# Optimization experiments

Hardware: AMD Instinct MI355X
Metric: run time of the kernel (lower is better)

Reference implementation:

```python
import jax, jax.numpy as jnp
from jax import lax
import numpy as np


def setup_inputs() -> dict:
    key = jax.random.key(0)
    ks = jax.random.split(key, 8)
    B, Cin, H, W = 4, 64, 128, 128
    D, N = 2 * Cin, 64  # D = in_ch*2, N = ssd_state_dim*2
    s = np.float32(1.0 / np.sqrt(D))
    return {
        "x": jax.random.normal(ks[0], (B, Cin, H, W), jnp.float32),
        "h_prev": jnp.zeros((B, D, N), jnp.float32),
        "norm_w": jnp.ones((D,), jnp.float32),
        "norm_b": jnp.zeros((D,), jnp.float32),
        "W_x": jax.random.normal(ks[1], (D, D), jnp.float32) * s,
        "W_B": jax.random.normal(ks[2], (N, D), jnp.float32) * s,
        "W_C": jax.random.normal(ks[3], (N, D), jnp.float32) * s,
        "w_dt": jax.random.normal(ks[4], (D,), jnp.float32) * s,
        "dt_bias": jnp.float32(0.0),
        "A_log": jnp.float32(0.0),
        "D_skip": jax.random.normal(ks[5], (D,), jnp.float32),
        "W_out": jax.random.normal(ks[6], (D, D), jnp.float32) * s,
    }


def _forward(x, h_prev, norm_w, norm_b, W_x, W_B, W_C, w_dt, dt_bias, A_log, D_skip, W_out):
    B, C, H, W = x.shape
    # rfft2 -> complex [B, C, Hf, Wf]
    xf = jnp.fft.rfft2(x, norm='ortho')
    Hf, Wf = xf.shape[-2], xf.shape[-1]
    L = Hf * Wf
    sqrt_n = jnp.sqrt(jnp.float32(H * W))
    # pack real/imag along channels: [B, 2C, L]
    u = jnp.concatenate([xf.real.reshape(B, C, L), xf.imag.reshape(B, C, L)], axis=1)
    # LayerNorm1D over the channel dim
    mu = jnp.mean(u, axis=1, keepdims=True)
    var = jnp.var(u, axis=1, keepdims=True)
    u = (u - mu) * lax.rsqrt(var + 1e-5) * norm_w[None, :, None] + norm_b[None, :, None]
    u = u / sqrt_n
    # SSD (Mamba2-style) recurrence over the L frequency tokens
    xs = jnp.einsum('ed,bdl->lbe', W_x, u)   # [L, B, D]
    Bs = jnp.einsum('nd,bdl->lbn', W_B, u)   # [L, B, N]
    Cs = jnp.einsum('nd,bdl->lbn', W_C, u)   # [L, B, N]
    dt = jax.nn.softplus(jnp.einsum('d,bdl->lb', w_dt, u) + dt_bias)  # [L, B]
    dec = jnp.exp(-jnp.exp(A_log) * dt)       # [L, B], A = -exp(A_log)

    def step(h, inp):
        x_t, B_t, C_t, dec_t, dt_t = inp
        h = dec_t[:, None, None] * h + (dt_t[:, None] * x_t)[:, :, None] * B_t[:, None, :]
        y_t = jnp.einsum('bdn,bn->bd', h, C_t)
        return h, y_t

    h_last, ys = lax.scan(step, h_prev, (xs, Bs, Cs, dec, dt))  # ys [L, B, D]
    y = ys.transpose(1, 2, 0) + D_skip[None, :, None] * xs.transpose(1, 2, 0)  # [B, D, L]
    freq_out = jnp.einsum('ed,bdl->bel', W_out, y) * sqrt_n
    # unpack real/imag halves and inverse FFT
    ft = (freq_out[:, :C] + 1j * freq_out[:, C:]).reshape(B, C, Hf, Wf)
    y_sp = jnp.fft.irfft2(ft, s=(H, W), norm='ortho')
    return y_sp, h_last


def reference(x, h_prev, norm_w, norm_b, W_x, W_B, W_C, w_dt, dt_bias, A_log, D_skip, W_out):
    return _forward(x, h_prev, norm_w, norm_b, W_x, W_B, W_C, w_dt, dt_bias, A_log, D_skip, W_out)
```

## Files before the change

kernel.cpp:

```cpp
#include <hip/hip_runtime.h>
#include <hip/hip_bf16.h>
#include <math.h>

#define BB 4
#define CC 64
#define HH 128
#define WW 128
#define DD 128
#define NN 64
#define HF 128
#define WF 65
#define LL 8320
#define TSEG 64
#define NSEG 130
#define PI2f 6.283185307179586f

__device__ __forceinline__ int brev7(int x) { return (int)(__brev((unsigned)x) >> 25); }

__global__ void k0_transpose(const float* __restrict__ Wx, const float* __restrict__ Wb,
                             const float* __restrict__ Wc, const float* __restrict__ Wout,
                             float* __restrict__ WcatT, float* __restrict__ WoT) {
  int idx = blockIdx.x * 256 + threadIdx.x;
  if (idx < 128 * 256) {
    int k = idx >> 8, o = idx & 255;
    float v;
    if (o < 128)      v = Wx[o * 128 + k];
    else if (o < 192) v = Wb[(o - 128) * 128 + k];
    else              v = Wc[(o - 192) * 128 + k];
    WcatT[k * 256 + o] = v;
  }
  if (idx < 128 * 128) {
    int d = idx >> 7, e = idx & 127;
    WoT[d * 128 + e] = Wout[e * 128 + d];
  }
}

__global__ __launch_bounds__(256) void k1_rfft(const float* __restrict__ x,
                                               float* __restrict__ T1) {
  __shared__ float2 data[128 * 17];
  __shared__ float2 tw[64];
  int tid = threadIdx.x;
  if (tid < 64) {
    float sv, cv;
    sincosf(PI2f * (float)tid * (1.f / 128.f), &sv, &cv);
    tw[tid] = make_float2(cv, sv);
  }
  int r0 = blockIdx.x * 32;
  const float* xp = x + (size_t)r0 * 128;
#pragma unroll
  for (int i = 0; i < 8; i++) {
    int e = i * 256 + tid;
    int p = e >> 7, j = e & 127;
    float v1 = xp[(2 * p) * 128 + j];
    float v2 = xp[(2 * p + 1) * 128 + j];
    data[brev7(j) * 17 + p] = make_float2(v1, v2);
  }
  __syncthreads();
  for (int s = 1; s <= 7; s++) {
    int half = 1 << (s - 1);
    int tsh = 7 - s;
#pragma unroll
    for (int i = 0; i < 4; i++) {
      int idx = i * 256 + tid;
      int t = idx >> 4, c = idx & 15;
      int j = t & (half - 1);
      int pos = ((t >> (s - 1)) << s) + j;
      float2 a = data[pos * 17 + c];
      float2 b = data[(pos + half) * 17 + c];
      float2 w = tw[j << tsh];
      float2 m = make_float2(b.x * w.x + b.y * w.y, b.y * w.x - b.x * w.y);
      data[pos * 17 + c] = make_float2(a.x + m.x, a.y + m.y);
      data[(pos + half) * 17 + c] = make_float2(a.x - m.x, a.y - m.y);
    }
    __syncthreads();
  }
  const float inv = 1.f / 128.f;
  float2* o = (float2*)T1 + (size_t)r0 * 65;
#pragma unroll
  for (int i = 0; i < 5; i++) {
    int e = i * 256 + tid;
    if (e < 1040) {
      int p = e / 65, k = e - p * 65;
      float2 Z = data[k * 17 + p];
      float2 Zc = data[((128 - k) & 127) * 17 + p];
      float2 X1 = make_float2((Z.x + Zc.x) * 0.5f * inv, (Z.y - Zc.y) * 0.5f * inv);
      float2 X2 = make_float2((Z.y + Zc.y) * 0.5f * inv, (Zc.x - Z.x) * 0.5f * inv);
      o[(2 * p) * 65 + k] = X1;
      o[(2 * p + 1) * 65 + k] = X2;
    }
  }
}

__global__ __launch_bounds__(256) void k2a_fft(const float* __restrict__ T1,
                                               float* __restrict__ uT) {
  __shared__ float2 data[128 * 34];
  __shared__ float2 tw[64];
  int tid = threadIdx.x;
  if (tid < 64) {
    float sv, cv;
    sincosf(PI2f * (float)tid * (1.f / 128.f), &sv, &cv);
    tw[tid] = make_float2(cv, sv);
  }
  int chunk = blockIdx.x & 1;
  int bc = blockIdx.x >> 1;
  int wf0 = chunk * 32;
  const float2* Tp = (const float2*)T1 + (size_t)bc * 8320;
#pragma unroll
  for (int i = 0; i < 17; i++) {
    int e = i * 256 + tid;
    if (e < 4224) {
      int j = e / 33;
      int c = e - j * 33;
      data[brev7(j) * 34 + c] = Tp[j * 65 + wf0 + c];
    }
  }
  __syncthreads();
  for (int s = 1; s <= 7; s++) {
    int half = 1 << (s - 1);
    int tsh = 7 - s;
#pragma unroll
    for (int i = 0; i < 9; i++) {
      int idx = i * 256 + tid;
      if (idx < 2112) {
        int t = idx / 33;
        int c = idx - t * 33;
        int j = t & (half - 1);
        int pos = ((t >> (s - 1)) << s) + j;
        float2 a = data[pos * 34 + c];
        float2 b = data[(pos + half) * 34 + c];
        float2 w = tw[j << tsh];
        float2 m = make_float2(b.x * w.x + b.y * w.y, b.y * w.x - b.x * w.y);
        data[pos * 34 + c] = make_float2(a.x + m.x, a.y + m.y);
        data[(pos + half) * 34 + c] = make_float2(a.x - m.x, a.y - m.y);
      }
    }
    __syncthreads();
  }
  int b = bc >> 6, ch = bc & 63;
  float* pr = uT + (size_t)(b * 128 + ch) * 8320;
  float* pi = uT + (size_t)(b * 128 + 64 + ch) * 8320;
#pragma unroll
  for (int i = 0; i < 17; i++) {
    int e = i * 256 + tid;
    if (e < 4224) {
      int hf = e / 33;
      int c = e - hf * 33;
      float2 v = data[hf * 34 + c];
      pr[hf * 65 + wf0 + c] = v.x;
      pi[hf * 65 + wf0 + c] = v.y;
    }
  }
}

__global__ __launch_bounds__(256) void k3_ln_proj(
    const float* __restrict__ uT, const float* __restrict__ WcatT,
    const float* __restrict__ nw, const float* __restrict__ nb,
    const float* __restrict__ wdt, const float* __restrict__ dtbias,
    float* __restrict__ xs, float* __restrict__ Bs, float* __restrict__ Cs,
    float* __restrict__ dtb) {
  __shared__ float su[128 * 65];
  __shared__ float snw[128], snb[128], swdt[128];
  int tid = threadIdx.x;
  int b = blockIdx.x / 130, tile = blockIdx.x % 130;
  int l0 = tile * 64;
  if (tid < 128) { snw[tid] = nw[tid]; snb[tid] = nb[tid]; swdt[tid] = wdt[tid]; }
  const float* up = uT + (size_t)b * 128 * 8320 + l0;
#pragma unroll
  for (int i = 0; i < 8; i++) {
    int e = i * 256 + tid;
    int d = e >> 4, q = e & 15;
    float4 v = *(const float4*)(up + (size_t)d * 8320 + q * 4);
    su[d * 65 + q * 4 + 0] = v.x; su[d * 65 + q * 4 + 1] = v.y;
    su[d * 65 + q * 4 + 2] = v.z; su[d * 65 + q * 4 + 3] = v.w;
  }
  __syncthreads();
  int t = tid >> 2, j = tid & 3;
  float vals[32];
  float s = 0.f, s2 = 0.f;
#pragma unroll
  for (int i = 0; i < 32; i++) {
    float v = su[(4 * i + j) * 65 + t];
    vals[i] = v; s += v; s2 += v * v;
  }
  s += __shfl_xor(s, 1, 64);  s += __shfl_xor(s, 2, 64);
  s2 += __shfl_xor(s2, 1, 64); s2 += __shfl_xor(s2, 2, 64);
  float mu = s * (1.f / 128.f);
  float var = s2 * (1.f / 128.f) - mu * mu;
  float rs = rsqrtf(var + 1e-5f);
  float raw = 0.f;
#pragma unroll
  for (int i = 0; i < 32; i++) {
    int k = 4 * i + j;
    float v = ((vals[i] - mu) * rs * snw[k] + snb[k]) * (1.f / 128.f);
    su[k * 65 + t] = v;
    raw = fmaf(v, swdt[k], raw);
  }
  raw += __shfl_xor(raw, 1, 64); raw += __shfl_xor(raw, 2, 64);
  if (j == 0) {
    float z = raw + dtbias[0];
    float sp = fmaxf(z, 0.f) + log1pf(expf(-fabsf(z)));
    dtb[b * LL + l0 + t] = sp;
  }
  __syncthreads();
  int wv = tid >> 6;
  int lane = tid & 63;
  int t0 = wv * 16;
  float acc[16][4];
#pragma unroll
  for (int i = 0; i < 16; i++)
#pragma unroll
    for (int r = 0; r < 4; r++) acc[i][r] = 0.f;
  const float4* W4 = (const float4*)WcatT;
  for (int k = 0; k < 128; k++) {
    float4 w = W4[k * 64 + lane];
    const float* sr = &su[k * 65 + t0];
#pragma unroll
    for (int i = 0; i < 16; i++) {
      float uk = sr[i];
      acc[i][0] = fmaf(w.x, uk, acc[i][0]);
      acc[i][1] = fmaf(w.y, uk, acc[i][1]);
      acc[i][2] = fmaf(w.z, uk, acc[i][2]);
      acc[i][3] = fmaf(w.w, uk, acc[i][3]);
    }
  }
  size_t tok0 = (size_t)b * LL + l0 + t0;
  float* basep;
  size_t stride;
  if (lane < 32)      { basep = xs + tok0 * 128 + lane * 4;        stride = 128; }
  else if (lane < 48) { basep = Bs + tok0 * 64 + (lane - 32) * 4;  stride = 64; }
  else                { basep = Cs + tok0 * 64 + (lane - 48) * 4;  stride = 64; }
#pragma unroll
  for (int i = 0; i < 16; i++)
    *(float4*)(basep + (size_t)i * stride) =
        make_float4(acc[i][0], acc[i][1], acc[i][2], acc[i][3]);
}

__global__ __launch_bounds__(256) void k5_seg(
    const float* __restrict__ xs, const float* __restrict__ Bs, const float* __restrict__ Cs,
    const float* __restrict__ dtb, const float* __restrict__ Alog,
    const float* __restrict__ Dskip,
    float* __restrict__ ybuf, float* __restrict__ Sseg, float* __restrict__ ssegb,
    float* __restrict__ cumg) {
  __shared__ __align__(16) float sX[64 * 128];
  __shared__ __align__(16) float sB[64 * 68];
  __shared__ __align__(16) float sCM[64 * 68];
  __shared__ float sdt[64], slc[64], sws[64];
  int tid = threadIdx.x;
  int b = blockIdx.x / NSEG, seg = blockIdx.x % NSEG;
  int tokbase = b * LL + seg * TSEG;
  const float4* xg = (const float4*)(xs + (size_t)tokbase * 128);
  float4* sX4 = (float4*)sX;
#pragma unroll
  for (int i = 0; i < 8; i++) sX4[i * 256 + tid] = xg[i * 256 + tid];
  const float4* bg = (const float4*)(Bs + (size_t)tokbase * 64);
  const float4* cg = (const float4*)(Cs + (size_t)tokbase * 64);
#pragma unroll
  for (int i = 0; i < 4; i++) {
    int e = i * 256 + tid;
    int t = e >> 4, n4 = e & 15;
    *(float4*)&sB[t * 68 + n4 * 4] = bg[e];
    *(float4*)&sCM[t * 68 + n4 * 4] = cg[e];
  }
  if (tid < 64) sdt[tid] = dtb[tokbase + tid];
  __syncthreads();
  if (tid < 64) {
    float a = expf(Alog[0]);
    float v = -a * sdt[tid];
#pragma unroll
    for (int off = 1; off < 64; off <<= 1) {
      float o = __shfl_up(v, off, 64);
      if (tid >= off) v += o;
    }
    slc[tid] = v;
    float l63 = __shfl(v, 63, 64);
    sws[tid] = expf(l63 - v) * sdt[tid];
    cumg[tokbase + tid] = expf(v);
    if (tid == 63) ssegb[seg * BB + b] = expf(v);
  }
  __syncthreads();
  int t0 = (tid >> 4) * 4, s0 = (tid & 15) * 4;
  float g[4][4];
#pragma unroll
  for (int i = 0; i < 4; i++)
#pragma unroll
    for (int j = 0; j < 4; j++) g[i][j] = 0.f;
  for (int n4 = 0; n4 < 16; n4++) {
    float4 cr[4], br[4];
#pragma unroll
    for (int i = 0; i < 4; i++) cr[i] = *(const float4*)&sCM[(t0 + i) * 68 + n4 * 4];
#pragma unroll
    for (int j = 0; j < 4; j++) br[j] = *(const float4*)&sB[(s0 + j) * 68 + n4 * 4];
#pragma unroll
    for (int i = 0; i < 4; i++)
#pragma unroll
      for (int j = 0; j < 4; j++) {
        g[i][j] = fmaf(cr[i].x, br[j].x, g[i][j]);
        g[i][j] = fmaf(cr[i].y, br[j].y, g[i][j]);
        g[i][j] = fmaf(cr[i].z, br[j].z, g[i][j]);
        g[i][j] = fmaf(cr[i].w, br[j].w, g[i][j]);
      }
  }
  __syncthreads();
#pragma unroll
  for (int i = 0; i < 4; i++) {
    int t = t0 + i;
    float4 m;
    float lt = slc[t];
    m.x = (s0 + 0 <= t) ? expf(lt - slc[s0 + 0]) * sdt[s0 + 0] * g[i][0] : 0.f;
    m.y = (s0 + 1 <= t) ? expf(lt - slc[s0 + 1]) * sdt[s0 + 1] * g[i][1] : 0.f;
    m.z = (s0 + 2 <= t) ? expf(lt - slc[s0 + 2]) * sdt[s0 + 2] * g[i][2] : 0.f;
    m.w = (s0 + 3 <= t) ? expf(lt - slc[s0 + 3]) * sdt[s0 + 3] * g[i][3] : 0.f;
    *(float4*)&sCM[t * 68 + s0] = m;
  }
  __syncthreads();
  int d0 = (tid & 15) * 8;
  {
    float acc[4][8];
#pragma unroll
    for (int i = 0; i < 4; i++)
#pragma unroll
      for (int j = 0; j < 8; j++) acc[i][j] = 0.f;
    for (int s = 0; s < 64; s++) {
      float4 x0 = *(const float4*)&sX[s * 128 + d0];
      float4 x1 = *(const float4*)&sX[s * 128 + d0 + 4];
      float xv[8] = {x0.x, x0.y, x0.z, x0.w, x1.x, x1.y, x1.z, x1.w};
#pragma unroll
      for (int i = 0; i < 4; i++) {
        float m = sCM[(t0 + i) * 68 + s];
#pragma unroll
        for (int j = 0; j < 8; j++) acc[i][j] = fmaf(m, xv[j], acc[i][j]);
      }
    }
    float4 dk0 = *(const float4*)&Dskip[d0];
    float4 dk1 = *(const float4*)&Dskip[d0 + 4];
    float dk[8] = {dk0.x, dk0.y, dk0.z, dk0.w, dk1.x, dk1.y, dk1.z, dk1.w};
#pragma unroll
    for (int i = 0; i < 4; i++) {
      int t = t0 + i;
      float4 x0 = *(const float4*)&sX[t * 128 + d0];
      float4 x1 = *(const float4*)&sX[t * 128 + d0 + 4];
      float xv[8] = {x0.x, x0.y, x0.z, x0.w, x1.x, x1.y, x1.z, x1.w};
      float4 y0, y1;
      y0.x = fmaf(dk[0], xv[0], acc[i][0]); y0.y = fmaf(dk[1], xv[1], acc[i][1]);
      y0.z = fmaf(dk[2], xv[2], acc[i][2]); y0.w = fmaf(dk[3], xv[3], acc[i][3]);
      y1.x = fmaf(dk[4], xv[4], acc[i][4]); y1.y = fmaf(dk[5], xv[5], acc[i][5]);
      y1.z = fmaf(dk[6], xv[6], acc[i][6]); y1.w = fmaf(dk[7], xv[7], acc[i][7]);
      float* yp = ybuf + (size_t)(tokbase + t) * 128 + d0;
      *(float4*)yp = y0;
      *(float4*)(yp + 4) = y1;
    }
  }
  {
    int dd0 = (tid >> 4) * 8, n0 = (tid & 15) * 4;
    float sacc[8][4];
#pragma unroll
    for (int k = 0; k < 8; k++)
#pragma unroll
      for (int j = 0; j < 4; j++) sacc[k][j] = 0.f;
    for (int s = 0; s < 64; s++) {
      float w = sws[s];
      float4 b4 = *(const float4*)&sB[s * 68 + n0];
      b4.x *= w; b4.y *= w; b4.z *= w; b4.w *= w;
      float4 x0 = *(const float4*)&sX[s * 128 + dd0];
      float4 x1 = *(const float4*)&sX[s * 128 + dd0 + 4];
      float xv[8] = {x0.x, x0.y, x0.z, x0.w, x1.x, x1.y, x1.z, x1.w};
#pragma unroll
      for (int k = 0; k < 8; k++) {
        sacc[k][0] = fmaf(xv[k], b4.x, sacc[k][0]);
        sacc[k][1] = fmaf(xv[k], b4.y, sacc[k][1]);
        sacc[k][2] = fmaf(xv[k], b4.z, sacc[k][2]);
        sacc[k][3] = fmaf(xv[k], b4.w, sacc[k][3]);
      }
    }
    float* Sp = Sseg + (size_t)seg * 32768 + (size_t)b * 8192;
#pragma unroll
    for (int k = 0; k < 8; k++)
      *(float4*)&Sp[(dd0 + k) * 64 + n0] =
          make_float4(sacc[k][0], sacc[k][1], sacc[k][2], sacc[k][3]);
  }
}

__global__ void k5b_states(const float* __restrict__ h_prev, const float* __restrict__ Sseg,
                           const float* __restrict__ ssegb, float* __restrict__ Hp,
                           float* __restrict__ h_last) {
  int gid = blockIdx.x * 256 + threadIdx.x;
  int b = gid >> 13;
  float h = h_prev[gid];
  for (int p = 0; p < NSEG; p++) {
    Hp[(size_t)p * 32768 + gid] = h;
    h = fmaf(ssegb[p * 4 + b], h, Sseg[(size_t)p * 32768 + gid]);
  }
  h_last[gid] = h;
}

__global__ __launch_bounds__(256) void k5c_correct(
    const float* __restrict__ Cs, const float* __restrict__ Hp,
    const float* __restrict__ cumg, float* __restrict__ ybuf) {
  __shared__ __align__(16) float Ct[64 * 64];
  __shared__ __align__(16) float Ht[64 * 132];
  __shared__ float cg[64];
  int tid = threadIdx.x;
  int b = blockIdx.x / NSEG, seg = blockIdx.x % NSEG;
  int tokbase = b * LL + seg * 64;
  const float* Csrc = Cs + (size_t)tokbase * 64;
#pragma unroll
  for (int i = 0; i < 16; i++) {
    int e = tid + i * 256;
    Ct[(e & 63) * 64 + (e >> 6)] = Csrc[e];
  }
  const float* Hsrc = Hp + (size_t)seg * 32768 + (size_t)b * 8192;
#pragma unroll
  for (int i = 0; i < 32; i++) {
    int e = tid + i * 256;
    Ht[(e & 63) * 132 + (e >> 6)] = Hsrc[e];
  }
  if (tid < 64) cg[tid] = cumg[tokbase + tid];
  __syncthreads();
  int og = tid & 15, tg = tid >> 4;
  int d0 = og * 8, t0 = tg * 4;
  float acc[4][8];
#pragma unroll
  for (int i = 0; i < 4; i++)
#pragma unroll
    for (int jj = 0; jj < 8; jj++) acc[i][jj] = 0.f;
  for (int n = 0; n < 64; n++) {
    float4 c4 = *(const float4*)&Ct[n * 64 + t0];
    float4 h0 = *(const float4*)&Ht[n * 132 + d0];
    float4 h1 = *(const float4*)&Ht[n * 132 + d0 + 4];
    float cv[4] = {c4.x, c4.y, c4.z, c4.w};
    float hv[8] = {h0.x, h0.y, h0.z, h0.w, h1.x, h1.y, h1.z, h1.w};
#pragma unroll
    for (int i = 0; i < 4; i++)
#pragma unroll
      for (int jj = 0; jj < 8; jj++) acc[i][jj] = fmaf(cv[i], hv[jj], acc[i][jj]);
  }
#pragma unroll
  for (int i = 0; i < 4; i++) {
    float sc = cg[t0 + i];
    float* yp = ybuf + (size_t)(tokbase + t0 + i) * 128 + d0;
    float4 y0 = *(float4*)yp;
    float4 y1 = *(float4*)(yp + 4);
    y0.x = fmaf(sc, acc[i][0], y0.x); y0.y = fmaf(sc, acc[i][1], y0.y);
    y0.z = fmaf(sc, acc[i][2], y0.z); y0.w = fmaf(sc, acc[i][3], y0.w);
    y1.x = fmaf(sc, acc[i][4], y1.x); y1.y = fmaf(sc, acc[i][5], y1.y);
    y1.z = fmaf(sc, acc[i][6], y1.z); y1.w = fmaf(sc, acc[i][7], y1.w);
    *(float4*)yp = y0; *(float4*)(yp + 4) = y1;
  }
}

__global__ __launch_bounds__(256) void k6_outproj(
    const float* __restrict__ ybuf, const float* __restrict__ WoT,
    float* __restrict__ T2) {
  __shared__ float sy[128 * 65];
  int tid = threadIdx.x;
  int b = blockIdx.x / 130, tile = blockIdx.x % 130;
  int l0 = tile * 64;
  const float* yg = ybuf + ((size_t)b * LL + l0) * 128;
#pragma unroll
  for (int i = 0; i < 8; i++) {
    int e = i * 256 + tid;
    int t = e >> 5, q = e & 31;
    float4 v = *(const float4*)(yg + t * 128 + q * 4);
    sy[(q * 4 + 0) * 65 + t] = v.x; sy[(q * 4 + 1) * 65 + t] = v.y;
    sy[(q * 4 + 2) * 65 + t] = v.z; sy[(q * 4 + 3) * 65 + t] = v.w;
  }
  __syncthreads();
  int wv = tid >> 6;
  int lane = tid & 63;
  int o4 = lane & 31, th = lane >> 5;
  int tt0 = wv * 16 + th * 8;
  float acc[8][4];
#pragma unroll
  for (int i = 0; i < 8; i++)
#pragma unroll
    for (int r = 0; r < 4; r++) acc[i][r] = 0.f;
  const float4* W4 = (const float4*)WoT;
  for (int k = 0; k < 128; k++) {
    float4 w = W4[k * 32 + o4];
    const float* sr = &sy[k * 65 + tt0];
#pragma unroll
    for (int i = 0; i < 8; i++) {
      float yk = sr[i];
      acc[i][0] = fmaf(w.x, yk, acc[i][0]);
      acc[i][1] = fmaf(w.y, yk, acc[i][1]);
      acc[i][2] = fmaf(w.z, yk, acc[i][2]);
      acc[i][3] = fmaf(w.w, yk, acc[i][3]);
    }
  }
#pragma unroll
  for (int i = 0; i < 8; i++) {
    int l = l0 + tt0 + i;
    *(float4*)(T2 + ((size_t)b * LL + l) * 128 + o4 * 4) =
        make_float4(acc[i][0] * 128.f, acc[i][1] * 128.f,
                    acc[i][2] * 128.f, acc[i][3] * 128.f);
  }
}

__global__ __launch_bounds__(256) void k7t_transpose(const float* __restrict__ T2,
                                                     float* __restrict__ T2T) {
  __shared__ __align__(16) float tile[32][132];
  int tid = threadIdx.x;
  int b = blockIdx.x / 260, lt = blockIdx.x % 260;
  int l0 = lt * 32;
#pragma unroll
  for (int i = 0; i < 4; i++) {
    int e = i * 256 + tid;
    int l = e >> 5, f4 = e & 31;
    float4 v = *(const float4*)(T2 + ((size_t)(b * LL + l0 + l)) * 128 + f4 * 4);
    *(float4*)&tile[l][f4 * 4] = v;
  }
  __syncthreads();
  int l = tid & 31, c2 = tid >> 5;
  float2* out = (float2*)T2T;
#pragma unroll
  for (int k = 0; k < 8; k++) {
    int c = c2 * 8 + k;
    float2 z = make_float2(tile[l][c], tile[l][64 + c]);
    out[((size_t)(b * 64 + c)) * 8320 + l0 + l] = z;
  }
}

__global__ __launch_bounds__(256) void k7a_fft(const float* __restrict__ T2T,
                                               float* __restrict__ TY) {
  __shared__ float2 data[128 * 34];
  __shared__ float2 tw[64];
  int tid = threadIdx.x;
  if (tid < 64) {
    float sv, cv;
    sincosf(PI2f * (float)tid * (1.f / 128.f), &sv, &cv);
    tw[tid] = make_float2(cv, sv);
  }
  int chunk = blockIdx.x & 1;
  int bc = blockIdx.x >> 1;
  int wf0 = chunk * 32;
  const float2* Zp = (const float2*)T2T + (size_t)bc * 8320;
#pragma unroll
  for (int i = 0; i < 17; i++) {
    int e = i * 256 + tid;
    if (e < 4224) {
      int j = e / 33;
      int c = e - j * 33;
      data[brev7(j) * 34 + c] = Zp[j * 65 + wf0 + c];
    }
  }
  __syncthreads();
  for (int s = 1; s <= 7; s++) {
    int half = 1 << (s - 1);
    int tsh = 7 - s;
#pragma unroll
    for (int i = 0; i < 9; i++) {
      int idx = i * 256 + tid;
      if (idx < 2112) {
        int t = idx / 33;
        int c = idx - t * 33;
        int j = t & (half - 1);
        int pos = ((t >> (s - 1)) << s) + j;
        float2 a = data[pos * 34 + c];
        float2 b = data[(pos + half) * 34 + c];
        float2 w = tw[j << tsh];
        float2 m = make_float2(b.x * w.x - b.y * w.y, b.y * w.x + b.x * w.y);
        data[pos * 34 + c] = make_float2(a.x + m.x, a.y + m.y);
        data[(pos + half) * 34 + c] = make_float2(a.x - m.x, a.y - m.y);
      }
    }
    __syncthreads();
  }
  float2* po = (float2*)TY + (size_t)bc * 8320;
#pragma unroll
  for (int i = 0; i < 17; i++) {
    int e = i * 256 + tid;
    if (e < 4224) {
      int h = e / 33;
      int c = e - h * 33;
      po[h * 65 + wf0 + c] = data[h * 34 + c];
    }
  }
}

__global__ __launch_bounds__(256) void k8_irfft(const float* __restrict__ TY,
                                                float* __restrict__ out) {
  __shared__ float2 zsh[32 * 66];
  __shared__ float2 data[128 * 17];
  __shared__ float2 tw[64];
  int tid = threadIdx.x;
  if (tid < 64) {
    float sv, cv;
    sincosf(PI2f * (float)tid * (1.f / 128.f), &sv, &cv);
    tw[tid] = make_float2(cv, sv);
  }
  int r0 = blockIdx.x * 32;
  const float2* Zp = (const float2*)TY + (size_t)r0 * 65;
#pragma unroll
  for (int i = 0; i < 9; i++) {
    int e = i * 256 + tid;
    if (e < 2080) {
      int r = e / 65, wf = e - r * 65;
      zsh[r * 66 + wf] = Zp[r * 65 + wf];
    }
  }
  __syncthreads();
#pragma unroll
  for (int i = 0; i < 8; i++) {
    int e = i * 256 + tid;
    int p = e >> 7, j = e & 127;
    int jj = (j <= 64) ? j : 128 - j;
    float2 a1 = zsh[(2 * p) * 66 + jj];
    float2 a2 = zsh[(2 * p + 1) * 66 + jj];
    if (jj == 0 || jj == 64) { a1.y = 0.f; a2.y = 0.f; }
    float2 V = (j <= 64) ? make_float2(a1.x - a2.y, a1.y + a2.x)
                         : make_float2(a1.x + a2.y, a2.x - a1.y);
    data[brev7(j) * 17 + p] = V;
  }
  __syncthreads();
  for (int s = 1; s <= 7; s++) {
    int half = 1 << (s - 1);
    int tsh = 7 - s;
#pragma unroll
    for (int i = 0; i < 4; i++) {
      int idx = i * 256 + tid;
      int t = idx >> 4, c = idx & 15;
      int j = t & (half - 1);
      int pos = ((t >> (s - 1)) << s) + j;
      float2 a = data[pos * 17 + c];
      float2 b = data[(pos + half) * 17 + c];
      float2 w = tw[j << tsh];
      float2 m = make_float2(b.x * w.x - b.y * w.y, b.y * w.x + b.x * w.y);
      data[pos * 17 + c] = make_float2(a.x + m.x, a.y + m.y);
      data[(pos + half) * 17 + c] = make_float2(a.x - m.x, a.y - m.y);
    }
    __syncthreads();
  }
  const float inv = 1.f / 128.f;
  float* op = out + (size_t)r0 * 128;
#pragma unroll
  for (int i = 0; i < 8; i++) {
    int e = i * 256 + tid;
    int p = e >> 7, w = e & 127;
    float2 X = data[w * 17 + p];
    op[(2 * p) * 128 + w] = X.x * inv;
    op[(2 * p + 1) * 128 + w] = X.y * inv;
  }
}

extern "C" void kernel_launch(void* const* d_in, const int* in_sizes, int n_in,
                              void* d_out, int out_size, void* d_ws, size_t ws_size,
                              hipStream_t stream) {
  const float* x      = (const float*)d_in[0];
  const float* h_prev = (const float*)d_in[1];
  const float* nw     = (const float*)d_in[2];
  const float* nb     = (const float*)d_in[3];
  const float* Wx     = (const float*)d_in[4];
  const float* Wb     = (const float*)d_in[5];
  const float* Wc     = (const float*)d_in[6];
  const float* wdt    = (const float*)d_in[7];
  const float* dtbias = (const float*)d_in[8];
  const float* Alog   = (const float*)d_in[9];
  const float* Dskip  = (const float*)d_in[10];
  const float* Wout   = (const float*)d_in[11];
  float* out = (float*)d_out;

  float* ws = (float*)d_ws;
  const size_t SZ_BIG = 4259840;
  const size_t SZ_BN  = 2129920;
  float* RA = ws;
  float* RB = RA + SZ_BIG;
  float* RC = RB + SZ_BIG;
  float* RD = RC + SZ_BIG;
  float* RE = RD + SZ_BN;
  float* dtb   = RE + SZ_BN;
  float* cumg  = dtb + 33280;
  float* ssegb = cumg + 33280;
  float* WcatT = ssegb + 520;
  float* WoT   = WcatT + 32768;

  hipLaunchKernelGGL(k0_transpose, dim3(128), dim3(256), 0, stream, Wx, Wb, Wc, Wout, WcatT, WoT);
  hipLaunchKernelGGL(k1_rfft, dim3(1024), dim3(256), 0, stream, x, RA );
  hipLaunchKernelGGL(k2a_fft, dim3(512), dim3(256), 0, stream, RA , RB );
  hipLaunchKernelGGL(k3_ln_proj, dim3(520), dim3(256), 0, stream,
                     RB , WcatT, nw, nb, wdt, dtbias, RA , RD , RE , dtb);
  hipLaunchKernelGGL(k5_seg, dim3(520), dim3(256), 0, stream,
                     RA , RD , RE , dtb, Alog, Dskip,
                     RB , RC , ssegb, cumg);
  hipLaunchKernelGGL(k5b_states, dim3(128), dim3(256), 0, stream,
                     h_prev, RC , ssegb, RA , out + 4194304);
  hipLaunchKernelGGL(k5c_correct, dim3(520), dim3(256), 0, stream,
                     RE , RA , cumg, RB );
  hipLaunchKernelGGL(k6_outproj, dim3(520), dim3(256), 0, stream, RB , WoT, RC );
  hipLaunchKernelGGL(k7t_transpose, dim3(1040), dim3(256), 0, stream, RC , RD );
  hipLaunchKernelGGL(k7a_fft, dim3(512), dim3(256), 0, stream, RD , RA );
  hipLaunchKernelGGL(k8_irfft, dim3(1024), dim3(256), 0, stream, RA , out);
}
```

Measured before the change: 212.6 us.

## Split segment kernel over D halves and vectorize shared-memory reads in projections

The segment-scan kernel now launches twice as many blocks, each handling half of the D channels, which halves per-block shared memory and register accumulators. The Gram matrix and decay computations are duplicated across the two halves in exchange for more parallelism across CUs. The LN-projection and out-projection kernels change their shared-memory padding from 65 to 68 floats so that inner-loop reads become float4 loads, and they add a min-blocks-per-CU launch bound of 2. The padding of 68 may bring back bank conflicts on transposed scalar accesses, and the duplicated Gram work adds compute.

Measured after the change: 211.8 us. About the same (-0.4%).

```diff
diff --git a/kernel.cpp b/kernel.cpp
--- a/kernel.cpp
+++ b/kernel.cpp
@@ -152,13 +152,13 @@
   }
 }
 
-__global__ __launch_bounds__(256) void k3_ln_proj(
+__global__ __launch_bounds__(256, 2) void k3_ln_proj(
     const float* __restrict__ uT, const float* __restrict__ WcatT,
     const float* __restrict__ nw, const float* __restrict__ nb,
     const float* __restrict__ wdt, const float* __restrict__ dtbias,
     float* __restrict__ xs, float* __restrict__ Bs, float* __restrict__ Cs,
     float* __restrict__ dtb) {
-  __shared__ float su[128 * 65];
+  __shared__ float su[128 * 68];
   __shared__ float snw[128], snb[128], swdt[128];
   int tid = threadIdx.x;
   int b = blockIdx.x / 130, tile = blockIdx.x % 130;
@@ -170,8 +170,7 @@
     int e = i * 256 + tid;
     int d = e >> 4, q = e & 15;
     float4 v = *(const float4*)(up + (size_t)d * 8320 + q * 4);
-    su[d * 65 + q * 4 + 0] = v.x; su[d * 65 + q * 4 + 1] = v.y;
-    su[d * 65 + q * 4 + 2] = v.z; su[d * 65 + q * 4 + 3] = v.w;
+    *(float4*)&su[d * 68 + q * 4] = v;
   }
   __syncthreads();
   int t = tid >> 2, j = tid & 3;
@@ -179,7 +178,7 @@
   float s = 0.f, s2 = 0.f;
 #pragma unroll
   for (int i = 0; i < 32; i++) {
-    float v = su[(4 * i + j) * 65 + t];
+    float v = su[(4 * i + j) * 68 + t];
     vals[i] = v; s += v; s2 += v * v;
   }
   s += __shfl_xor(s, 1, 64);  s += __shfl_xor(s, 2, 64);
@@ -192,7 +191,7 @@
   for (int i = 0; i < 32; i++) {
     int k = 4 * i + j;
     float v = ((vals[i] - mu) * rs * snw[k] + snb[k]) * (1.f / 128.f);
-    su[k * 65 + t] = v;
+    su[k * 68 + t] = v;
     raw = fmaf(v, swdt[k], raw);
   }
   raw += __shfl_xor(raw, 1, 64); raw += __shfl_xor(raw, 2, 64);
@@ -213,14 +212,16 @@
   const float4* W4 = (const float4*)WcatT;
   for (int k = 0; k < 128; k++) {
     float4 w = W4[k * 64 + lane];
-    const float* sr = &su[k * 65 + t0];
+    const float4* sr4 = (const float4*)&su[k * 68 + t0];
+    float4 u0 = sr4[0], u1 = sr4[1], u2 = sr4[2], u3 = sr4[3];
+    float uk[16] = {u0.x, u0.y, u0.z, u0.w, u1.x, u1.y, u1.z, u1.w,
+                    u2.x, u2.y, u2.z, u2.w, u3.x, u3.y, u3.z, u3.w};
 #pragma unroll
     for (int i = 0; i < 16; i++) {
-      float uk = sr[i];
-      acc[i][0] = fmaf(w.x, uk, acc[i][0]);
-      acc[i][1] = fmaf(w.y, uk, acc[i][1]);
-      acc[i][2] = fmaf(w.z, uk, acc[i][2]);
-      acc[i][3] = fmaf(w.w, uk, acc[i][3]);
+      acc[i][0] = fmaf(w.x, uk[i], acc[i][0]);
+      acc[i][1] = fmaf(w.y, uk[i], acc[i][1]);
+      acc[i][2] = fmaf(w.z, uk[i], acc[i][2]);
+      acc[i][3] = fmaf(w.w, uk[i], acc[i][3]);
     }
   }
   size_t tok0 = (size_t)b * LL + l0 + t0;
@@ -241,17 +242,22 @@
     const float* __restrict__ Dskip,
     float* __restrict__ ybuf, float* __restrict__ Sseg, float* __restrict__ ssegb,
     float* __restrict__ cumg) {
-  __shared__ __align__(16) float sX[64 * 128];
+  __shared__ __align__(16) float sX[64 * 68];
   __shared__ __align__(16) float sB[64 * 68];
   __shared__ __align__(16) float sCM[64 * 68];
   __shared__ float sdt[64], slc[64], sws[64];
   int tid = threadIdx.x;
-  int b = blockIdx.x / NSEG, seg = blockIdx.x % NSEG;
+  int half = blockIdx.x & 1;
+  int bs = blockIdx.x >> 1;
+  int b = bs / NSEG, seg = bs % NSEG;
   int tokbase = b * LL + seg * TSEG;
   const float4* xg = (const float4*)(xs + (size_t)tokbase * 128);
-  float4* sX4 = (float4*)sX;
-#pragma unroll
-  for (int i = 0; i < 8; i++) sX4[i * 256 + tid] = xg[i * 256 + tid];
+#pragma unroll
+  for (int i = 0; i < 4; i++) {
+    int e = i * 256 + tid;
+    int t = e >> 4, q = e & 15;
+    *(float4*)&sX[t * 68 + q * 4] = xg[t * 32 + half * 16 + q];
+  }
   const float4* bg = (const float4*)(Bs + (size_t)tokbase * 64);
   const float4* cg = (const float4*)(Cs + (size_t)tokbase * 64);
 #pragma unroll
@@ -274,8 +280,10 @@
     slc[tid] = v;
     float l63 = __shfl(v, 63, 64);
     sws[tid] = expf(l63 - v) * sdt[tid];
-    cumg[tokbase + tid] = expf(v);
-    if (tid == 63) ssegb[seg * BB + b] = expf(v);
+    if (half == 0) {
+      cumg[tokbase + tid] = expf(v);
+      if (tid == 63) ssegb[seg * BB + b] = expf(v);
+    }
   }
   __syncthreads();
   int t0 = (tid >> 4) * 4, s0 = (tid & 15) * 4;
@@ -313,69 +321,62 @@
     *(float4*)&sCM[t * 68 + s0] = m;
   }
   __syncthreads();
-  int d0 = (tid & 15) * 8;
   {
-    float acc[4][8];
+    int d0 = (tid & 15) * 4;
+    float acc[4][4];
 #pragma unroll
     for (int i = 0; i < 4; i++)
 #pragma unroll
-      for (int j = 0; j < 8; j++) acc[i][j] = 0.f;
+      for (int j = 0; j < 4; j++) acc[i][j] = 0.f;
     for (int s = 0; s < 64; s++) {
-      float4 x0 = *(const float4*)&sX[s * 128 + d0];
-      float4 x1 = *(const float4*)&sX[s * 128 + d0 + 4];
-      float xv[8] = {x0.x, x0.y, x0.z, x0.w, x1.x, x1.y, x1.z, x1.w};
+      float4 xv = *(const float4*)&sX[s * 68 + d0];
 #pragma unroll
       for (int i = 0; i < 4; i++) {
         float m = sCM[(t0 + i) * 68 + s];
-#pragma unroll
-        for (int j = 0; j < 8; j++) acc[i][j] = fmaf(m, xv[j], acc[i][j]);
+        acc[i][0] = fmaf(m, xv.x, acc[i][0]);
+        acc[i][1] = fmaf(m, xv.y, acc[i][1]);
+        acc[i][2] = fmaf(m, xv.z, acc[i][2]);
+        acc[i][3] = fmaf(m, xv.w, acc[i][3]);
       }
     }
-    float4 dk0 = *(const float4*)&Dskip[d0];
-    float4 dk1 = *(const float4*)&Dskip[d0 + 4];
-    float dk[8] = {dk0.x, dk0.y, dk0.z, dk0.w, dk1.x, dk1.y, dk1.z, dk1.w};
+    float4 dk = *(const float4*)&Dskip[half * 64 + d0];
 #pragma unroll
     for (int i = 0; i < 4; i++) {
       int t = t0 + i;
-      float4 x0 = *(const float4*)&sX[t * 128 + d0];
-      float4 x1 = *(const float4*)&sX[t * 128 + d0 + 4];
-      float xv[8] = {x0.x, x0.y, x0.z, x0.w, x1.x, x1.y, x1.z, x1.w};
-      float4 y0, y1;
-      y0.x = fmaf(dk[0], xv[0], acc[i][0]); y0.y = fmaf(dk[1], xv[1], acc[i][1]);
-      y0.z = fmaf(dk[2], xv[2], acc[i][2]); y0.w = fmaf(dk[3], xv[3], acc[i][3]);
-      y1.x = fmaf(dk[4], xv[4], acc[i][4]); y1.y = fmaf(dk[5], xv[5], acc[i][5]);
-      y1.z = fmaf(dk[6], xv[6], acc[i][6]); y1.w = fmaf(dk[7], xv[7], acc[i][7]);
-      float* yp = ybuf + (size_t)(tokbase + t) * 128 + d0;
-      *(float4*)yp = y0;
-      *(float4*)(yp + 4) = y1;
+      float4 xv = *(const float4*)&sX[t * 68 + d0];
+      float4 y;
+      y.x = fmaf(dk.x, xv.x, acc[i][0]);
+      y.y = fmaf(dk.y, xv.y, acc[i][1]);
+      y.z = fmaf(dk.z, xv.z, acc[i][2]);
+      y.w = fmaf(dk.w, xv.w, acc[i][3]);
+      *(float4*)(ybuf + (size_t)(tokbase + t) * 128 + half * 64 + d0) = y;
     }
   }
   {
-    int dd0 = (tid >> 4) * 8, n0 = (tid & 15) * 4;
-    float sacc[8][4];
-#pragma unroll
-    for (int k = 0; k < 8; k++)
+    int dd0 = (tid >> 4) * 4, n0 = (tid & 15) * 4;
+    float sacc[4][4];
+#pragma unroll
+    for (int k = 0; k < 4; k++)
 #pragma unroll
       for (int j = 0; j < 4; j++) sacc[k][j] = 0.f;
     for (int s = 0; s < 64; s++) {
       float w = sws[s];
       float4 b4 = *(const float4*)&sB[s * 68 + n0];
       b4.x *= w; b4.y *= w; b4.z *= w; b4.w *= w;
-      float4 x0 = *(const float4*)&sX[s * 128 + dd0];
-      float4 x1 = *(const float4*)&sX[s * 128 + dd0 + 4];
-      float xv[8] = {x0.x, x0.y, x0.z, x0.w, x1.x, x1.y, x1.z, x1.w};
-#pragma unroll
-      for (int k = 0; k < 8; k++) {
-        sacc[k][0] = fmaf(xv[k], b4.x, sacc[k][0]);
-        sacc[k][1] = fmaf(xv[k], b4.y, sacc[k][1]);
-        sacc[k][2] = fmaf(xv[k], b4.z, sacc[k][2]);
-        sacc[k][3] = fmaf(xv[k], b4.w, sacc[k][3]);
+      float4 xv = *(const float4*)&sX[s * 68 + dd0];
+      float xk[4] = {xv.x, xv.y, xv.z, xv.w};
+#pragma unroll
+      for (int k = 0; k < 4; k++) {
+        sacc[k][0] = fmaf(xk[k], b4.x, sacc[k][0]);
+        sacc[k][1] = fmaf(xk[k], b4.y, sacc[k][1]);
+        sacc[k][2] = fmaf(xk[k], b4.z, sacc[k][2]);
+        sacc[k][3] = fmaf(xk[k], b4.w, sacc[k][3]);
       }
     }
     float* Sp = Sseg + (size_t)seg * 32768 + (size_t)b * 8192;
 #pragma unroll
-    for (int k = 0; k < 8; k++)
-      *(float4*)&Sp[(dd0 + k) * 64 + n0] =
+    for (int k = 0; k < 4; k++)
+      *(float4*)&Sp[(half * 64 + dd0 + k) * 64 + n0] =
           make_float4(sacc[k][0], sacc[k][1], sacc[k][2], sacc[k][3]);
   }
 }
@@ -448,10 +449,10 @@
   }
 }
 
-__global__ __launch_bounds__(256) void k6_outproj(
+__global__ __launch_bounds__(256, 2) void k6_outproj(
     const float* __restrict__ ybuf, const float* __restrict__ WoT,
     float* __restrict__ T2) {
-  __shared__ float sy[128 * 65];
+  __shared__ float sy[128 * 68];
   int tid = threadIdx.x;
   int b = blockIdx.x / 130, tile = blockIdx.x % 130;
   int l0 = tile * 64;
@@ -461,8 +462,8 @@
     int e = i * 256 + tid;
     int t = e >> 5, q = e & 31;
     float4 v = *(const float4*)(yg + t * 128 + q * 4);
-    sy[(q * 4 + 0) * 65 + t] = v.x; sy[(q * 4 + 1) * 65 + t] = v.y;
-    sy[(q * 4 + 2) * 65 + t] = v.z; sy[(q * 4 + 3) * 65 + t] = v.w;
+    sy[(q * 4 + 0) * 68 + t] = v.x; sy[(q * 4 + 1) * 68 + t] = v.y;
+    sy[(q * 4 + 2) * 68 + t] = v.z; sy[(q * 4 + 3) * 68 + t] = v.w;
   }
   __syncthreads();
   int wv = tid >> 6;
@@ -477,14 +478,15 @@
   const float4* W4 = (const float4*)WoT;
   for (int k = 0; k < 128; k++) {
     float4 w = W4[k * 32 + o4];
-    const float* sr = &sy[k * 65 + tt0];
+    const float4* sr4 = (const float4*)&sy[k * 68 + tt0];
+    float4 u0 = sr4[0], u1 = sr4[1];
+    float yk[8] = {u0.x, u0.y, u0.z, u0.w, u1.x, u1.y, u1.z, u1.w};
 #pragma unroll
     for (int i = 0; i < 8; i++) {
-      float yk = sr[i];
-      acc[i][0] = fmaf(w.x, yk, acc[i][0]);
-      acc[i][1] = fmaf(w.y, yk, acc[i][1]);
-      acc[i][2] = fmaf(w.z, yk, acc[i][2]);
-      acc[i][3] = fmaf(w.w, yk, acc[i][3]);
+      acc[i][0] = fmaf(w.x, yk[i], acc[i][0]);
+      acc[i][1] = fmaf(w.y, yk[i], acc[i][1]);
+      acc[i][2] = fmaf(w.z, yk[i], acc[i][2]);
+      acc[i][3] = fmaf(w.w, yk[i], acc[i][3]);
     }
   }
 #pragma unroll
@@ -678,7 +680,7 @@
   hipLaunchKernelGGL(k2a_fft, dim3(512), dim3(256), 0, stream, RA , RB );
   hipLaunchKernelGGL(k3_ln_proj, dim3(520), dim3(256), 0, stream,
                      RB , WcatT, nw, nb, wdt, dtbias, RA , RD , RE , dtb);
-  hipLaunchKernelGGL(k5_seg, dim3(520), dim3(256), 0, stream,
+  hipLaunchKernelGGL(k5_seg, dim3(1040), dim3(256), 0, stream,
                      RA , RD , RE , dtb, Alog, Dskip,
                      RB , RC , ssegb, cumg);
   hipLaunchKernelGGL(k5b_states, dim3(128), dim3(256), 0, stream,
```
